# Optimization experiments

Measured on AMD Instinct MI355X. Metric: run time of the kernel, lower is better.

Reference implementation:

```python
import jax, jax.numpy as jnp
import numpy as np


def _sign(x):
    # sign(r) = 1 if r > 0 else -1 (matches 2*(r>0)-1 in the torch code)
    return 2.0 * (x > 0).astype(x.dtype) - 1.0


def setup_inputs() -> dict:
    key = jax.random.key(0)
    k1, k2 = jax.random.split(key)
    x = jax.random.normal(k1, (32, 256, 56, 56), dtype=jnp.float32)
    weight = jax.random.normal(k2, (256, 256, 3, 3), dtype=jnp.float32)
    alpha = jnp.ones((256, 1, 1), dtype=jnp.float32)
    return {"x": x, "weight": weight, "alpha": alpha}


def reference(x, weight, alpha):
    # conv2d(sign(x), sign(W), stride=1, padding=1) * alpha
    out = jax.lax.conv_general_dilated(
        _sign(x), _sign(weight),
        window_strides=(1, 1),
        padding=[(1, 1), (1, 1)],
        dimension_numbers=("NCHW", "OIHW", "NCHW"),
    )
    return out * alpha  # alpha: (C_out, 1, 1) broadcasts over (N, C_out, H, W)
```

## Files before the change

### kernel.cpp

```cpp
#include <hip/hip_runtime.h>
#include <stdint.h>

typedef unsigned long long u64;

#define CIN    256
#define COUT   256
#define HW     56
#define NPIX   (HW * HW)
#define PADW   58
#define PPIX   (PADW * PADW)
#define NBATCH 32

__global__ __launch_bounds__(256) void pack_x_kernel(const float* __restrict__ x,
                                                     u64* __restrict__ xb) {
    int p = blockIdx.x * 256 + threadIdx.x;
    int n = blockIdx.y;
    int q = blockIdx.z;
    if (p >= NPIX) return;
    const float* xp = x + ((size_t)(n * CIN + q * 64)) * NPIX + p;
    u64 word = 0;
#pragma unroll
    for (int j = 0; j < 64; ++j) {
        word |= (u64)(xp[(size_t)j * NPIX] > 0.0f) << j;
    }
    int h = p / HW, w = p % HW;
    xb[((size_t)n * PPIX + (size_t)(h + 1) * PADW + (w + 1)) * 4 + q] = word;
}

__global__ __launch_bounds__(64) void packw_ab_kernel(const float* __restrict__ wt,
                                                      const float* __restrict__ alpha,
                                                      u64* __restrict__ wb,
                                                      float* __restrict__ A,
                                                      float* __restrict__ B) {
    int co   = blockIdx.x;
    int lane = threadIdx.x;
    u64 myword = 0;
    int kpop[9];
#pragma unroll
    for (int k = 0; k < 9; ++k) {
        int kp = 0;
#pragma unroll
        for (int q = 0; q < 4; ++q) {
            float v = wt[((size_t)(co * CIN + q * 64 + lane)) * 9 + k];
            u64 mask = __ballot(v > 0.0f);
            kp += __popcll(mask);
            if (lane == k * 4 + q) myword = mask;
        }
        kpop[k] = kp;
    }
    if (lane < 36) wb[(size_t)co * 36 + lane] = myword;
    float al = alpha[co];
    if (lane == 0) B[co] = 2.0f * al;
    if (lane < 9) {
        int ch = lane / 3, cw = lane % 3;
        int wcl = 0, vcnt = 0;
#pragma unroll
        for (int k = 0; k < 9; ++k) {
            int kh = k / 3, kw = k % 3;
            bool inv = (kh == 0 && ch == 0) || (kh == 2 && ch == 2) ||
                       (kw == 0 && cw == 0) || (kw == 2 && cw == 2);
            if (inv) wcl += kpop[k]; else vcnt++;
        }
        A[co * 9 + lane] = al * (float)(256 * vcnt + 2 * wcl);
    }
}

__global__ __launch_bounds__(256, 4) void conv_kernel(const u64* __restrict__ xb,
                                                      const u64* __restrict__ wb,
                                                      const float* __restrict__ A,
                                                      const float* __restrict__ B,
                                                      float* __restrict__ out) {
    int tid   = threadIdx.x;
    int ptile = blockIdx.x;
    int n     = blockIdx.y;
    int chunk = blockIdx.z;
    int p = ptile * 256 + tid;
    if (p >= NPIX) return;
    int h = p / HW, w = p % HW;

    u64 xn[9][4];
    const u64* xbase = xb + ((size_t)n * PPIX + (size_t)h * PADW + w) * 4;
#pragma unroll
    for (int dh = 0; dh < 3; ++dh)
#pragma unroll
        for (int dw = 0; dw < 3; ++dw)
#pragma unroll
            for (int q = 0; q < 4; ++q)
                xn[dh * 3 + dw][q] = xbase[((size_t)dh * PADW + dw) * 4 + q];

    int ch  = (h == 0) ? 0 : ((h == HW - 1) ? 2 : 1);
    int cw  = (w == 0) ? 0 : ((w == HW - 1) ? 2 : 1);
    int cls = ch * 3 + cw;

    int co0 = chunk * 64;
    const u64*   wp = wb + (size_t)co0 * 36;
    float*       op = out + ((size_t)(n * COUT + co0)) * NPIX + p;
    const float* Ap = A + co0 * 9 + cls;
    const float* Bp = B + co0;

    for (int c = 0; c < 64; ++c) {
        int acc[4] = {0, 0, 0, 0};
#pragma unroll
        for (int k = 0; k < 9; ++k) {
#pragma unroll
            for (int q = 0; q < 4; ++q) {
                acc[q] += __popcll(xn[k][q] ^ wp[k * 4 + q]);
            }
        }
        int pc = (acc[0] + acc[1]) + (acc[2] + acc[3]);
        op[0] = Ap[c * 9] - Bp[c] * (float)pc;
        op += NPIX;
        wp += 36;
    }
}

extern "C" void kernel_launch(void* const* d_in, const int* in_sizes, int n_in,
                              void* d_out, int out_size, void* d_ws, size_t ws_size,
                              hipStream_t stream) {
    const float* x     = (const float*)d_in[0];
    const float* wt    = (const float*)d_in[1];
    const float* alpha = (const float*)d_in[2];
    float* out = (float*)d_out;

    char* ws = (char*)d_ws;
    u64* xb = (u64*)ws;
    size_t xb_bytes = (size_t)NBATCH * PPIX * 4 * sizeof(u64);
    u64* wb = (u64*)(ws + xb_bytes);
    size_t wb_bytes = (size_t)COUT * 9 * 4 * sizeof(u64);
    float* A = (float*)(ws + xb_bytes + wb_bytes);
    float* B = A + COUT * 9;

    hipMemsetAsync(xb, 0, xb_bytes, stream);

    pack_x_kernel<<<dim3(13, NBATCH, 4), 256, 0, stream>>>(x, xb);
    packw_ab_kernel<<<dim3(COUT), 64, 0, stream>>>(wt, alpha, wb, A, B);
    conv_kernel<<<dim3(13, NBATCH, 4), 256, 0, stream>>>(xb, wb, A, B, out);
}
```

Baseline: 309.6 us.

## Replace XNOR-popcount conv with int8 MFMA implicit GEMM using LDS double buffering

Encodes signs as int8 values (+1/-1) instead of bit-packed words and computes the binary convolution as an implicit GEMM with 32x32x32 int8 MFMA instructions. Weight and activation tiles are streamed into LDS with global_load_lds and double buffered across the 72 k-steps. Padding is written as zeros into a padded layout, so the border-correction terms and the memset are no longer needed. This trades 8x more input bytes than the bit-packed form for matrix-core throughput instead of scalar popcount work.

```diff
diff --git a/kernel.cpp b/kernel.cpp
--- a/kernel.cpp
+++ b/kernel.cpp
@@ -1,116 +1,138 @@
 #include <hip/hip_runtime.h>
 #include <stdint.h>
 
-typedef unsigned long long u64;
+typedef int i32x4  __attribute__((ext_vector_type(4)));
+typedef int i32x16 __attribute__((ext_vector_type(16)));
 
+#define HW     56
+#define NPIX   3136
+#define PADW   58
+#define PPIX   3364
+#define NB     32
 #define CIN    256
 #define COUT   256
-#define HW     56
-#define NPIX   (HW * HW)
-#define PADW   58
-#define PPIX   (PADW * PADW)
-#define NBATCH 32
+#define STRW   32
+#define ROWB   (PADW*STRW)
+#define GSTR   (PPIX*STRW)
+#define NSTR   (8*GSTR)
+#define NKID   72
 
-__global__ __launch_bounds__(256) void pack_x_kernel(const float* __restrict__ x,
-                                                     u64* __restrict__ xb) {
-    int p = blockIdx.x * 256 + threadIdx.x;
-    int n = blockIdx.y;
-    int q = blockIdx.z;
-    if (p >= NPIX) return;
-    const float* xp = x + ((size_t)(n * CIN + q * 64)) * NPIX + p;
-    u64 word = 0;
+__global__ __launch_bounds__(256) void pack_x(const float* __restrict__ x,
+                                              char* __restrict__ xsp) {
+    int pp = blockIdx.x * 256 + threadIdx.x;
+    if (pp >= PPIX) return;
+    int n = blockIdx.y, g = blockIdx.z;
+    int hh = pp / PADW, ww = pp % PADW;
+    char* dst = xsp + (size_t)n * NSTR + (size_t)g * GSTR + (size_t)pp * STRW;
+    unsigned int wd[8];
+    if (hh == 0 || hh == PADW - 1 || ww == 0 || ww == PADW - 1) {
 #pragma unroll
-    for (int j = 0; j < 64; ++j) {
-        word |= (u64)(xp[(size_t)j * NPIX] > 0.0f) << j;
+        for (int m = 0; m < 8; ++m) wd[m] = 0u;
+    } else {
+        const float* xp = x + ((size_t)(n * CIN + g * 32)) * NPIX
+                            + (size_t)(hh - 1) * HW + (ww - 1);
+#pragma unroll
+        for (int m = 0; m < 8; ++m) {
+            unsigned int v = 0;
+#pragma unroll
+            for (int jj = 0; jj < 4; ++jj) {
+                unsigned int b = (xp[(size_t)(m * 4 + jj) * NPIX] > 0.0f) ? 0x01u : 0xFFu;
+                v |= b << (8 * jj);
+            }
+            wd[m] = v;
+        }
     }
-    int h = p / HW, w = p % HW;
-    xb[((size_t)n * PPIX + (size_t)(h + 1) * PADW + (w + 1)) * 4 + q] = word;
+    ((i32x4*)dst)[0] = *(i32x4*)&wd[0];
+    ((i32x4*)dst)[1] = *(i32x4*)&wd[4];
 }
 
-__global__ __launch_bounds__(64) void packw_ab_kernel(const float* __restrict__ wt,
-                                                      const float* __restrict__ alpha,
-                                                      u64* __restrict__ wb,
-                                                      float* __restrict__ A,
-                                                      float* __restrict__ B) {
-    int co   = blockIdx.x;
-    int lane = threadIdx.x;
-    u64 myword = 0;
-    int kpop[9];
+__global__ __launch_bounds__(256) void pack_w(const float* __restrict__ wt,
+                                              char* __restrict__ wsp) {
+    int b  = blockIdx.x;
+    int co = threadIdx.x;
+    int g  = b / 9, r = b % 9;
+    const float* wp = wt + ((size_t)co * CIN + g * 32) * 9 + r;
 #pragma unroll
-    for (int k = 0; k < 9; ++k) {
-        int kp = 0;
+    for (int s = 0; s < 2; ++s) {
+        unsigned int wd[4];
 #pragma unroll
-        for (int q = 0; q < 4; ++q) {
-            float v = wt[((size_t)(co * CIN + q * 64 + lane)) * 9 + k];
-            u64 mask = __ballot(v > 0.0f);
-            kp += __popcll(mask);
-            if (lane == k * 4 + q) myword = mask;
+        for (int m = 0; m < 4; ++m) {
+            unsigned int v = 0;
+#pragma unroll
+            for (int jj = 0; jj < 4; ++jj) {
+                unsigned int bb = (wp[(size_t)(s * 16 + m * 4 + jj) * 9] > 0.0f) ? 0x01u : 0xFFu;
+                v |= bb << (8 * jj);
+            }
+            wd[m] = v;
         }
-        kpop[k] = kp;
-    }
-    if (lane < 36) wb[(size_t)co * 36 + lane] = myword;
-    float al = alpha[co];
-    if (lane == 0) B[co] = 2.0f * al;
-    if (lane < 9) {
-        int ch = lane / 3, cw = lane % 3;
-        int wcl = 0, vcnt = 0;
-#pragma unroll
-        for (int k = 0; k < 9; ++k) {
-            int kh = k / 3, kw = k % 3;
-            bool inv = (kh == 0 && ch == 0) || (kh == 2 && ch == 2) ||
-                       (kw == 0 && cw == 0) || (kw == 2 && cw == 2);
-            if (inv) wcl += kpop[k]; else vcnt++;
-        }
-        A[co * 9 + lane] = al * (float)(256 * vcnt + 2 * wcl);
+        *(i32x4*)(wsp + ((size_t)(b * 2 + s) * COUT + co) * 16) = *(i32x4*)wd;
     }
 }
 
-__global__ __launch_bounds__(256, 4) void conv_kernel(const u64* __restrict__ xb,
-                                                      const u64* __restrict__ wb,
-                                                      const float* __restrict__ A,
-                                                      const float* __restrict__ B,
-                                                      float* __restrict__ out) {
+__device__ inline void gload16(const void* g, void* l) {
+    __builtin_amdgcn_global_load_lds(
+        (const __attribute__((address_space(1))) unsigned int*)g,
+        (__attribute__((address_space(3))) unsigned int*)l, 16, 0, 0);
+}
+
+__global__ __launch_bounds__(256, 2) void conv_mfma(const char* __restrict__ xsp,
+                                                    const char* __restrict__ wsp,
+                                                    const float* __restrict__ alpha,
+                                                    float* __restrict__ out) {
+    __shared__ char lA[2][4096];
+    __shared__ char lB[2][4096];
     int tid   = threadIdx.x;
     int ptile = blockIdx.x;
-    int n     = blockIdx.y;
-    int chunk = blockIdx.z;
-    int p = ptile * 256 + tid;
-    if (p >= NPIX) return;
-    int h = p / HW, w = p % HW;
+    int mtile = blockIdx.y;
+    int t7 = tid >> 7, t127 = tid & 127;
 
-    u64 xn[9][4];
-    const u64* xbase = xb + ((size_t)n * PPIX + (size_t)h * PADW + w) * 4;
+    size_t aoff = (size_t)t7 * 4096 + (size_t)(mtile * 128 + t127) * 16;
+    int pix = ptile * 128 + t127;
+    int n = pix / NPIX, pq = pix % NPIX;
+    int h = pq / HW, w = pq % HW;
+    size_t boff = (size_t)n * NSTR + (size_t)h * ROWB + (size_t)w * STRW + (size_t)t7 * 16;
+
+    i32x16 acc[4] = {};
+
+    gload16(wsp + aoff, &lA[0][tid * 16]);
+    gload16(xsp + boff, &lB[0][tid * 16]);
+    __syncthreads();
+
+    int l = tid & 63, wv = tid >> 6;
+    int s2048  = (l >> 5) * 2048;
+    int l31_16 = (l & 31) * 16;
+
+    for (int k = 0; k < NKID; ++k) {
+        int buf = k & 1;
+        if (k < NKID - 1) {
+            int kn = k + 1;
+            int g = kn / 9, r = kn % 9, kh = r / 3, kw = r % 3;
+            gload16(wsp + (size_t)kn * 8192 + aoff, &lA[buf ^ 1][tid * 16]);
+            gload16(xsp + boff + (size_t)g * GSTR + (size_t)kh * ROWB + (size_t)kw * STRW,
+                    &lB[buf ^ 1][tid * 16]);
+        }
+        i32x4 bfrag = *(const i32x4*)&lB[buf][s2048 + wv * 512 + l31_16];
+        i32x4 af[4];
 #pragma unroll
-    for (int dh = 0; dh < 3; ++dh)
+        for (int mi = 0; mi < 4; ++mi)
+            af[mi] = *(const i32x4*)&lA[buf][s2048 + mi * 512 + l31_16];
 #pragma unroll
-        for (int dw = 0; dw < 3; ++dw)
+        for (int mi = 0; mi < 4; ++mi)
+            acc[mi] = __builtin_amdgcn_mfma_i32_32x32x32_i8(af[mi], bfrag, acc[mi], 0, 0, 0);
+        __syncthreads();
+    }
+
+    int hi = l >> 5;
+    int pixo = ptile * 128 + wv * 32 + (l & 31);
+    int on = pixo / NPIX, opp = pixo % NPIX;
+    float* ob = out + (size_t)on * COUT * NPIX + opp;
 #pragma unroll
-            for (int q = 0; q < 4; ++q)
-                xn[dh * 3 + dw][q] = xbase[((size_t)dh * PADW + dw) * 4 + q];
-
-    int ch  = (h == 0) ? 0 : ((h == HW - 1) ? 2 : 1);
-    int cw  = (w == 0) ? 0 : ((w == HW - 1) ? 2 : 1);
-    int cls = ch * 3 + cw;
-
-    int co0 = chunk * 64;
-    const u64*   wp = wb + (size_t)co0 * 36;
-    float*       op = out + ((size_t)(n * COUT + co0)) * NPIX + p;
-    const float* Ap = A + co0 * 9 + cls;
-    const float* Bp = B + co0;
-
-    for (int c = 0; c < 64; ++c) {
-        int acc[4] = {0, 0, 0, 0};
+    for (int mi = 0; mi < 4; ++mi) {
 #pragma unroll
-        for (int k = 0; k < 9; ++k) {
-#pragma unroll
-            for (int q = 0; q < 4; ++q) {
-                acc[q] += __popcll(xn[k][q] ^ wp[k * 4 + q]);
-            }
+        for (int r = 0; r < 16; ++r) {
+            int co = mtile * 128 + mi * 32 + (r & 3) + 8 * (r >> 2) + 4 * hi;
+            ob[(size_t)co * NPIX] = alpha[co] * (float)acc[mi][r];
         }
-        int pc = (acc[0] + acc[1]) + (acc[2] + acc[3]);
-        op[0] = Ap[c * 9] - Bp[c] * (float)pc;
-        op += NPIX;
-        wp += 36;
     }
 }
 
@@ -122,17 +144,11 @@
     const float* alpha = (const float*)d_in[2];
     float* out = (float*)d_out;
 
-    char* ws = (char*)d_ws;
-    u64* xb = (u64*)ws;
-    size_t xb_bytes = (size_t)NBATCH * PPIX * 4 * sizeof(u64);
-    u64* wb = (u64*)(ws + xb_bytes);
-    size_t wb_bytes = (size_t)COUT * 9 * 4 * sizeof(u64);
-    float* A = (float*)(ws + xb_bytes + wb_bytes);
-    float* B = A + COUT * 9;
+    char* ws  = (char*)d_ws;
+    char* xsp = ws;
+    char* wsp = ws + (size_t)NB * NSTR;
 
-    hipMemsetAsync(xb, 0, xb_bytes, stream);
-
-    pack_x_kernel<<<dim3(13, NBATCH, 4), 256, 0, stream>>>(x, xb);
-    packw_ab_kernel<<<dim3(COUT), 64, 0, stream>>>(wt, alpha, wb, A, B);
-    conv_kernel<<<dim3(13, NBATCH, 4), 256, 0, stream>>>(xb, wb, A, B, out);
+    pack_x<<<dim3(14, NB, 8), 256, 0, stream>>>(x, xsp);
+    pack_w<<<dim3(NKID), 256, 0, stream>>>(wt, wsp);
+    conv_mfma<<<dim3(784, 2), 256, 0, stream>>>(xsp, wsp, alpha, out);
 }
```

New measurement: 265.9 us. 14.1% less time.
